# Kernel optimization log

Measured on AMD Instinct MI355X. Metric: run time of the kernel, lower is better.

## Reference

```python
import jax, jax.numpy as jnp
import numpy as np

H = W = 512
IN_DIM = 3
WIDTH = 64
N_LAYERS = 4
M1 = M2 = 20
FC_DIM = 128
OUT_DIM = 1


def setup_inputs() -> dict:
    key = jax.random.key(0)
    ks = jax.random.split(key, 12)
    s = 1.0 / (WIDTH * WIDTH)
    return {
        "x": jax.random.normal(ks[0], (H, W, IN_DIM), jnp.float32),
        "fc0_w": jax.random.normal(ks[1], (WIDTH, IN_DIM), jnp.float32) * 0.1,
        "fc0_b": jnp.zeros((WIDTH,), jnp.float32),
        "sw1_r": jax.random.normal(ks[2], (N_LAYERS, WIDTH, WIDTH, M1, M2), jnp.float32) * s,
        "sw1_i": jax.random.normal(ks[3], (N_LAYERS, WIDTH, WIDTH, M1, M2), jnp.float32) * s,
        "sw2_r": jax.random.normal(ks[4], (N_LAYERS, WIDTH, WIDTH, M1, M2), jnp.float32) * s,
        "sw2_i": jax.random.normal(ks[5], (N_LAYERS, WIDTH, WIDTH, M1, M2), jnp.float32) * s,
        "conv_w": jax.random.normal(ks[6], (N_LAYERS, WIDTH, WIDTH), jnp.float32) * 0.1,
        "conv_b": jnp.zeros((N_LAYERS, WIDTH), jnp.float32),
        "fc1_w": jax.random.normal(ks[7], (FC_DIM, WIDTH), jnp.float32) * 0.1,
        "fc1_b": jnp.zeros((FC_DIM,), jnp.float32),
        "fc2_w": jax.random.normal(ks[8], (OUT_DIM, FC_DIM), jnp.float32) * 0.1,
        "fc2_b": jnp.zeros((OUT_DIM,), jnp.float32),
    }


def _spectral_conv(v, w1, w2):
    # v: (C, H, W); w1, w2: (C_in, C_out, M1, M2) complex64
    xf = jnp.fft.rfft2(v)  # (C, H, W//2+1) complex64
    out_ft = jnp.zeros((w1.shape[1], H, W // 2 + 1), jnp.complex64)
    top = jnp.einsum("ixy,ioxy->oxy", xf[:, :M1, :M2], w1)
    bot = jnp.einsum("ixy,ioxy->oxy", xf[:, -M1:, :M2], w2)
    out_ft = out_ft.at[:, :M1, :M2].set(top).at[:, -M1:, :M2].set(bot)
    return jnp.fft.irfft2(out_ft, s=(H, W))


def reference(x, fc0_w, fc0_b, sw1_r, sw1_i, sw2_r, sw2_i, conv_w, conv_b,
              fc1_w, fc1_b, fc2_w, fc2_b):
    v = jnp.transpose(x, (2, 0, 1))  # (in_dim, H, W)
    # fc0 applied pointwise over the grid (double_vmap Linear on channel axis)
    v = jnp.einsum("chw,oc->ohw", v, fc0_w) + fc0_b[:, None, None]
    for i in range(N_LAYERS):
        w1 = (sw1_r[i] + 1j * sw1_i[i]).astype(jnp.complex64)
        w2 = (sw2_r[i] + 1j * sw2_i[i]).astype(jnp.complex64)
        x1 = _spectral_conv(v, w1, w2)
        x2 = jnp.einsum("chw,oc->ohw", v, conv_w[i]) + conv_b[i][:, None, None]
        v = jnp.tanh(x1 + x2)
    v = jnp.tanh(jnp.einsum("chw,oc->ohw", v, fc1_w) + fc1_b[:, None, None])
    v = jnp.einsum("chw,oc->ohw", v, fc2_w) + fc2_b[:, None, None]
    return jnp.transpose(v, (1, 2, 0))  # (H, W, out_dim)
```

## Files before the change

### kernel.cpp

```cpp
#include <hip/hip_runtime.h>
#include <math.h>

typedef unsigned short u16;
typedef __attribute__((ext_vector_type(8))) short short8;
typedef __attribute__((ext_vector_type(8))) short bf16x8;
typedef __attribute__((ext_vector_type(4))) unsigned short us4;
typedef __attribute__((ext_vector_type(2))) unsigned short us2;
typedef __attribute__((ext_vector_type(4))) float f32x4;

#define NP (512*512)
#define MFMA16 __builtin_amdgcn_mfma_f32_16x16x32_bf16

#define TWH   0u
#define TWL   49152u
#define T2H   98304u
#define T2L   163840u
#define THC2H 229376u
#define THC2L 278528u
#define THS2H 327680u
#define THS2L 376832u
#define THCAH 425984u
#define THCAL 491520u
#define THSAH 557056u
#define THSAL 622592u
#define THSNH 688128u
#define THSNL 753664u
#define CFH   819200u
#define CFL   851968u
#define F1H   884736u
#define F1L   901120u
#define XWH   917504u
#define XWL   4063232u
#define XFP   7208960u
#define YPART 8028160u
#define YRH   8847360u
#define YRL   9011200u
#define YIH   9175040u
#define YIL   9338880u
#define ZH    9502720u
#define ZL    13697024u
#define VH    17891328u
#define VL    51445760u

__device__ __forceinline__ u16 brnd(float x){
    unsigned u = __float_as_uint(x);
    unsigned r = (u + 0x7FFFu + ((u>>16)&1u)) >> 16;
    return (u16)r;
}
__device__ __forceinline__ float fbf(u16 h){ return __uint_as_float(((unsigned)h)<<16); }
__device__ __forceinline__ void bsplit(float x, u16& h, u16& l){
    h = brnd(x); l = brnd(x - fbf(h));
}
__device__ __forceinline__ float tanhfast(float x){
    x = fminf(10.f, fmaxf(-10.f, x));
    float e = __expf(2.f*x);
    return (e-1.f)/(e+1.f);
}

__global__ void k_tables(char* wsb){
    int i = blockIdx.x*256 + threadIdx.x;
    const float c2pi = 6.283185307179586f/512.0f;
    if (i < 24576){
        int e=i&7, lane=(i>>3)&63, g=i>>9; int nt=g%3;
        int k = (g/3)*32 + ((lane>>4)<<3) + e;
        int n = nt*16 + (lane&15);
        float v=0.f;
        if(n<40){int kx=n>>1; float a=c2pi*(float)((kx*k)&511); v=(n&1)?-sinf(a):cosf(a);}
        u16 h,l; bsplit(v,h,l);
        ((u16*)(wsb+TWH))[i]=h; ((u16*)(wsb+TWL))[i]=l;
    } else if (i < 57344){
        int j2=i-24576;
        int e=j2&7, lane=(j2>>3)&63, g=j2>>9; int ks=g&1, wt=g>>1;
        int j = ks*32 + ((lane>>4)<<3) + e;
        int w = wt*16 + (lane&15);
        float v=0.f;
        if(j<40){int kx=j>>1; float a=c2pi*(float)((kx*w)&511); v=(j&1)?-sinf(a):cosf(a);}
        u16 h,l; bsplit(v,h,l);
        ((u16*)(wsb+T2H))[j2]=h; ((u16*)(wsb+T2L))[j2]=l;
    } else if (i < 81920){
        int j2 = i-57344;
        int m=j2>>9, hh=j2&511;
        float vc=0.f,vs=0.f;
        if(m<40){int ky=(m<20)?m:(472+m); float a=c2pi*(float)((ky*hh)&511); vc=cosf(a); vs=sinf(a);}
        u16 h,l;
        bsplit(vc,h,l); ((u16*)(wsb+THC2H))[j2]=h; ((u16*)(wsb+THC2L))[j2]=l;
        bsplit(vs,h,l); ((u16*)(wsb+THS2H))[j2]=h; ((u16*)(wsb+THS2L))[j2]=l;
    } else if (i < 114688){
        int j2 = i-81920;
        int hh=j2>>6, m=j2&63;
        float vc=0.f,vs=0.f;
        if(m<40){int ky=(m<20)?m:(472+m); float a=c2pi*(float)((ky*hh)&511); vc=cosf(a); vs=sinf(a);}
        u16 h,l;
        bsplit(vc,h,l);  ((u16*)(wsb+THCAH))[j2]=h; ((u16*)(wsb+THCAL))[j2]=l;
        bsplit(vs,h,l);  ((u16*)(wsb+THSAH))[j2]=h; ((u16*)(wsb+THSAL))[j2]=l;
        bsplit(-vs,h,l); ((u16*)(wsb+THSNH))[j2]=h; ((u16*)(wsb+THSNL))[j2]=l;
    }
}

__global__ void k_wprep(const float* __restrict__ convw, const float* __restrict__ fc1w, char* wsb){
    int i = blockIdx.x*256 + threadIdx.x;
    if (i < 16384){
        int e=i&7, lane=(i>>3)&63, g=i>>9;
        int mt=g&3, ks=(g>>2)&1, L=g>>3;
        int o = mt*16+(lane&15), c = ks*32+((lane>>4)<<3)+e;
        float v = convw[L*4096 + o*64 + c];
        u16 h,l; bsplit(v,h,l);
        ((u16*)(wsb+CFH))[i]=h; ((u16*)(wsb+CFL))[i]=l;
    } else if (i < 24576){
        int j2=i-16384;
        int e=j2&7, lane=(j2>>3)&63, g=j2>>9;
        int mt=g&7, ks=g>>3;
        int f = mt*16+(lane&15), c = ks*32+((lane>>4)<<3)+e;
        float v = fc1w[f*64+c];
        u16 h,l; bsplit(v,h,l);
        ((u16*)(wsb+F1H))[j2]=h; ((u16*)(wsb+F1L))[j2]=l;
    }
}

__global__ __launch_bounds__(256) void k_fc0(const float* __restrict__ x,
    const float* __restrict__ w, const float* __restrict__ b,
    u16* __restrict__ vh, u16* __restrict__ vl){
    __shared__ float xs[1024*3];
    __shared__ float ws3[192], bs[64];
    int t = threadIdx.x;
    size_t pb = (size_t)blockIdx.x*1024;
    const float4* xg = (const float4*)(x + pb*3);
    float4* xs4 = (float4*)xs;
    #pragma unroll
    for (int k=0;k<3;k++) xs4[t + k*256] = xg[t + k*256];
    if (t<192) ws3[t]=w[t];
    if (t<64) bs[t]=b[t];
    __syncthreads();
    int p0 = t*4;
    float X0[4],X1[4],X2[4];
    #pragma unroll
    for(int e=0;e<4;e++){X0[e]=xs[(p0+e)*3];X1[e]=xs[(p0+e)*3+1];X2[e]=xs[(p0+e)*3+2];}
    for (int c=0;c<64;c++){
        float w0=ws3[c*3],w1=ws3[c*3+1],w2=ws3[c*3+2],bc=bs[c];
        us4 sh, sl;
        #pragma unroll
        for(int e=0;e<4;e++){
            float v = w0*X0[e]+w1*X1[e]+w2*X2[e]+bc;
            u16 hh,ll; bsplit(v,hh,ll); sh[e]=hh; sl[e]=ll;
        }
        *(us4*)(vh + (size_t)c*NP + pb + p0) = sh;
        *(us4*)(vl + (size_t)c*NP + pb + p0) = sl;
    }
}

__global__ __launch_bounds__(256) void k_f1(const u16* __restrict__ vh, const u16* __restrict__ vl,
    const u16* __restrict__ twh, const u16* __restrict__ twl,
    u16* __restrict__ xwh, u16* __restrict__ xwl){
    int lane = threadIdx.x & 63, wv = threadIdx.x >> 6;
    int rowa = blockIdx.x*64 + wv*16 + (lane&15);
    const u16* ah = vh + (size_t)rowa*512 + ((lane>>4)<<3);
    const u16* al = vl + (size_t)rowa*512 + ((lane>>4)<<3);
    f32x4 acc[3];
    #pragma unroll
    for (int nt = 0; nt < 3; ++nt) acc[nt] = (f32x4){0.f,0.f,0.f,0.f};
    for (int kk = 0; kk < 16; ++kk){
        bf16x8 Ah = *reinterpret_cast<const bf16x8*>(ah + kk*32);
        bf16x8 Al = *reinterpret_cast<const bf16x8*>(al + kk*32);
        #pragma unroll
        for (int nt = 0; nt < 3; ++nt){
            size_t bo = ((size_t)(kk*3+nt)*64 + lane)*8;
            bf16x8 Bh = *reinterpret_cast<const bf16x8*>(twh + bo);
            bf16x8 Bl = *reinterpret_cast<const bf16x8*>(twl + bo);
            acc[nt] = MFMA16(Ah, Bh, acc[nt], 0,0,0);
            acc[nt] = MFMA16(Ah, Bl, acc[nt], 0,0,0);
            acc[nt] = MFMA16(Al, Bh, acc[nt], 0,0,0);
        }
    }
    int r0 = blockIdx.x*64 + wv*16 + ((lane>>4)<<2);
    int c = r0>>9, h0 = r0&511;
    int colj = lane&15;
    #pragma unroll
    for (int nt = 0; nt < 3; ++nt){
        int j = nt*16 + colj;
        us4 uh, ul;
        #pragma unroll
        for (int rg = 0; rg < 4; ++rg){
            u16 hh,ll; bsplit(acc[nt][rg],hh,ll); uh[rg]=hh; ul[rg]=ll;
        }
        size_t off = ((size_t)j*64 + c)*512 + h0;
        *(us4*)(xwh + off) = uh;
        *(us4*)(xwl + off) = ul;
    }
}

__global__ __launch_bounds__(256) void k_f2(const char* __restrict__ wsb, float* __restrict__ xfP){
    int b = blockIdx.x; int kx = b>>1, kh = b&1;
    int lane = threadIdx.x&63, wv = threadIdx.x>>6;
    const u16* thch=(const u16*)(wsb+THC2H); const u16* thcl=(const u16*)(wsb+THC2L);
    const u16* thsh=(const u16*)(wsb+THS2H); const u16* thsl=(const u16*)(wsb+THS2L);
    const u16* xwh=(const u16*)(wsb+XWH);   const u16* xwl=(const u16*)(wsb+XWL);
    f32x4 aA[3],aB[3],aC[3],aD[3];
    #pragma unroll
    for(int mt=0;mt<3;mt++){aA[mt]=(f32x4){0,0,0,0};aB[mt]=aA[mt];aC[mt]=aA[mt];aD[mt]=aA[mt];}
    int g8 = (lane>>4)<<3;
    int mrow = lane&15;
    int cB = wv*16 + (lane&15);
    size_t bre = ((size_t)(2*kx)*64 + cB)*512;
    size_t bim = ((size_t)(2*kx+1)*64 + cB)*512;
    for (int kk = kh*8; kk < kh*8+8; ++kk){
        int hof = kk*32 + g8;
        bf16x8 XRh = *reinterpret_cast<const bf16x8*>(xwh + bre + hof);
        bf16x8 XRl = *reinterpret_cast<const bf16x8*>(xwl + bre + hof);
        bf16x8 XIh = *reinterpret_cast<const bf16x8*>(xwh + bim + hof);
        bf16x8 XIl = *reinterpret_cast<const bf16x8*>(xwl + bim + hof);
        #pragma unroll
        for (int mt=0;mt<3;mt++){
            size_t ao = (size_t)(mt*16+mrow)*512 + hof;
            bf16x8 Ch = *reinterpret_cast<const bf16x8*>(thch+ao);
            bf16x8 Cl = *reinterpret_cast<const bf16x8*>(thcl+ao);
            bf16x8 Sh = *reinterpret_cast<const bf16x8*>(thsh+ao);
            bf16x8 Sl = *reinterpret_cast<const bf16x8*>(thsl+ao);
            aA[mt]=MFMA16(Ch,XRh,aA[mt],0,0,0); aA[mt]=MFMA16(Ch,XRl,aA[mt],0,0,0); aA[mt]=MFMA16(Cl,XRh,aA[mt],0,0,0);
            aB[mt]=MFMA16(Sh,XIh,aB[mt],0,0,0); aB[mt]=MFMA16(Sh,XIl,aB[mt],0,0,0); aB[mt]=MFMA16(Sl,XIh,aB[mt],0,0,0);
            aC[mt]=MFMA16(Ch,XIh,aC[mt],0,0,0); aC[mt]=MFMA16(Ch,XIl,aC[mt],0,0,0); aC[mt]=MFMA16(Cl,XIh,aC[mt],0,0,0);
            aD[mt]=MFMA16(Sh,XRh,aD[mt],0,0,0); aD[mt]=MFMA16(Sh,XRl,aD[mt],0,0,0); aD[mt]=MFMA16(Sl,XRh,aD[mt],0,0,0);
        }
    }
    #pragma unroll
    for (int mt=0;mt<3;mt++)
        #pragma unroll
        for (int rg=0;rg<4;rg++){
            int m = mt*16 + ((lane>>4)<<2) + rg;
            if (m < 40){
                float re = aA[mt][rg]+aB[mt][rg];
                float im = aC[mt][rg]-aD[mt][rg];
                size_t xo = ((size_t)kh*64 + cB)*1600 + (size_t)(m*20+kx)*2;
                xfP[xo] = re; xfP[xo+1] = im;
            }
        }
}

__global__ __launch_bounds__(256) void k_mix(const float* __restrict__ w1r,const float* __restrict__ w1i,
    const float* __restrict__ w2r,const float* __restrict__ w2i,
    const float* __restrict__ xfP, float* __restrict__ ypart){
    __shared__ float xs[2][800];
    int b = blockIdx.x;
    int iseg = b>>7, half = (b>>6)&1, o = b&63;
    int t = threadIdx.x;
    const float* wr = (half? w2r : w1r) + o*400;
    const float* wi = (half? w2i : w1i) + o*400;
    const float* xp0 = xfP + half*800;
    const float* xp1 = xfP + (size_t)64*1600 + half*800;
    int i0 = iseg*32;
    {
        const float* a = xp0 + (size_t)i0*1600; const float* c = xp1 + (size_t)i0*1600;
        xs[0][t]=a[t]+c[t]; xs[0][t+256]=a[t+256]+c[t+256];
        if (t<288) xs[0][t+512]=a[t+512]+c[t+512];
    }
    int p1 = t, p2 = t+256; bool has2 = (p2<400);
    float ar1=0,ai1=0,ar2=0,ai2=0;
    size_t wof = (size_t)i0*25600;
    float wAr1=wr[wof+p1], wAi1=wi[wof+p1];
    float wAr2=0,wAi2=0;
    if(has2){ wAr2=wr[wof+p2]; wAi2=wi[wof+p2]; }
    __syncthreads();
    for (int ii=0; ii<32; ++ii){
        int cur = ii&1;
        if (ii<31){
            int i = i0+ii+1;
            const float* a = xp0 + (size_t)i*1600; const float* c = xp1 + (size_t)i*1600;
            float* d = xs[cur^1];
            d[t]=a[t]+c[t]; d[t+256]=a[t+256]+c[t+256];
            if(t<288) d[t+512]=a[t+512]+c[t+512];
        }
        float wBr1=0,wBi1=0,wBr2=0,wBi2=0;
        if (ii<31){
            size_t wo2 = (size_t)(i0+ii+1)*25600;
            wBr1=wr[wo2+p1]; wBi1=wi[wo2+p1];
            if(has2){ wBr2=wr[wo2+p2]; wBi2=wi[wo2+p2]; }
        }
        float xr=xs[cur][2*p1], xi=xs[cur][2*p1+1];
        ar1 += xr*wAr1 - xi*wAi1; ai1 += xr*wAi1 + xi*wAr1;
        if (has2){
            float xr2=xs[cur][2*p2], xi2=xs[cur][2*p2+1];
            ar2 += xr2*wAr2 - xi2*wAi2; ai2 += xr2*wAi2 + xi2*wAr2;
        }
        wAr1=wBr1; wAi1=wBi1; wAr2=wBr2; wAi2=wBi2;
        __syncthreads();
    }
    int mode1 = half*400 + p1;
    size_t y1 = ((size_t)(iseg*800 + mode1)*64 + o)*2;
    ypart[y1]=ar1; ypart[y1+1]=ai1;
    if (has2){
        int mode2 = half*400 + p2;
        size_t y2 = ((size_t)(iseg*800 + mode2)*64 + o)*2;
        ypart[y2]=ar2; ypart[y2+1]=ai2;
    }
}

__global__ void k_mixred(const float* __restrict__ ypart, char* wsb){
    int g = blockIdx.x*256+threadIdx.x;
    int m = g&63, o=(g>>6)&63, kx=g>>12;
    float vr=0.f, vi=0.f;
    if (m<40){
        int mode = m*20+kx;
        size_t i0 = ((size_t)mode*64+o)*2;
        size_t i1 = ((size_t)(800+mode)*64+o)*2;
        float sc = (kx==0?1.f:2.f)*(1.f/262144.f);
        vr = (ypart[i0]+ypart[i1])*sc;
        vi = (ypart[i0+1]+ypart[i1+1])*sc;
    }
    u16 h,l; size_t yo = ((size_t)kx*64+o)*64+m;
    bsplit(vr,h,l); ((u16*)(wsb+YRH))[yo]=h; ((u16*)(wsb+YRL))[yo]=l;
    bsplit(vi,h,l); ((u16*)(wsb+YIH))[yo]=h; ((u16*)(wsb+YIL))[yo]=l;
}

__global__ __launch_bounds__(256) void k_i1(const char* __restrict__ wsb,
    u16* __restrict__ zh, u16* __restrict__ zl){
    int b = blockIdx.x; int kx = b>>3, hb = b&7;
    int lane = threadIdx.x&63, wv = threadIdx.x>>6;
    const u16* thcAh=(const u16*)(wsb+THCAH); const u16* thcAl=(const u16*)(wsb+THCAL);
    const u16* thsAh=(const u16*)(wsb+THSAH); const u16* thsAl=(const u16*)(wsb+THSAL);
    const u16* thsnh=(const u16*)(wsb+THSNH); const u16* thsnl=(const u16*)(wsb+THSNL);
    const u16* yrh=(const u16*)(wsb+YRH); const u16* yrl=(const u16*)(wsb+YRL);
    const u16* yih=(const u16*)(wsb+YIH); const u16* yil=(const u16*)(wsb+YIL);
    f32x4 aR[4], aI[4];
    #pragma unroll
    for(int nt=0;nt<4;nt++){aR[nt]=(f32x4){0,0,0,0}; aI[nt]=aR[nt];}
    int g8 = (lane>>4)<<3;
    int hrow = hb*64 + wv*16 + (lane&15);
    #pragma unroll
    for (int ks=0; ks<2; ++ks){
        size_t ao = (size_t)hrow*64 + ks*32 + g8;
        bf16x8 Ch=*reinterpret_cast<const bf16x8*>(thcAh+ao);
        bf16x8 Cl=*reinterpret_cast<const bf16x8*>(thcAl+ao);
        bf16x8 Sh=*reinterpret_cast<const bf16x8*>(thsAh+ao);
        bf16x8 Sl=*reinterpret_cast<const bf16x8*>(thsAl+ao);
        bf16x8 Nh=*reinterpret_cast<const bf16x8*>(thsnh+ao);
        bf16x8 Nl=*reinterpret_cast<const bf16x8*>(thsnl+ao);
        #pragma unroll
        for (int nt=0; nt<4; ++nt){
            int o = nt*16+(lane&15);
            size_t bo = ((size_t)kx*64+o)*64 + ks*32 + g8;
            bf16x8 Rh=*reinterpret_cast<const bf16x8*>(yrh+bo);
            bf16x8 Rl=*reinterpret_cast<const bf16x8*>(yrl+bo);
            bf16x8 Ih=*reinterpret_cast<const bf16x8*>(yih+bo);
            bf16x8 Il=*reinterpret_cast<const bf16x8*>(yil+bo);
            aR[nt]=MFMA16(Ch,Rh,aR[nt],0,0,0); aR[nt]=MFMA16(Ch,Rl,aR[nt],0,0,0); aR[nt]=MFMA16(Cl,Rh,aR[nt],0,0,0);
            aR[nt]=MFMA16(Nh,Ih,aR[nt],0,0,0); aR[nt]=MFMA16(Nh,Il,aR[nt],0,0,0); aR[nt]=MFMA16(Nl,Ih,aR[nt],0,0,0);
            aI[nt]=MFMA16(Sh,Rh,aI[nt],0,0,0); aI[nt]=MFMA16(Sh,Rl,aI[nt],0,0,0); aI[nt]=MFMA16(Sl,Rh,aI[nt],0,0,0);
            aI[nt]=MFMA16(Ch,Ih,aI[nt],0,0,0); aI[nt]=MFMA16(Ch,Il,aI[nt],0,0,0); aI[nt]=MFMA16(Cl,Ih,aI[nt],0,0,0);
        }
    }
    #pragma unroll
    for (int nt=0;nt<4;nt++)
        #pragma unroll
        for (int rg=0;rg<4;rg++){
            int h = hb*64 + wv*16 + ((lane>>4)<<2) + rg;
            int o = nt*16+(lane&15);
            size_t za = ((size_t)h*64+o)*64 + 2*kx;
            u16 h1,l1,h2,l2;
            bsplit(aR[nt][rg],h1,l1); bsplit(aI[nt][rg],h2,l2);
            us2 sh={h1,h2}, sl={l1,l2};
            *(us2*)(zh+za)=sh; *(us2*)(zl+za)=sl;
        }
}

#define SWZ(c,p) ((c) ^ (((p)&7)<<3))
__global__ __launch_bounds__(256) void k_sct(u16* __restrict__ vh, u16* __restrict__ vl,
    const char* __restrict__ wsb, int L, const float* __restrict__ cb,
    const u16* __restrict__ zh, const u16* __restrict__ zl){
    __shared__ u16 sh_[4096];
    __shared__ u16 sl_[4096];
    int t = threadIdx.x, lane = t&63, wv = t>>6;
    int h = blockIdx.x>>3, pb = (blockIdx.x&7)<<6;
    size_t gbase = (size_t)h*512 + pb;
    {
        int c = t>>2, p0=(t&3)<<4;
        short8 a0 = *(const short8*)(vh + (size_t)c*NP + gbase + p0);
        short8 a1 = *(const short8*)(vh + (size_t)c*NP + gbase + p0+8);
        short8 b0 = *(const short8*)(vl + (size_t)c*NP + gbase + p0);
        short8 b1 = *(const short8*)(vl + (size_t)c*NP + gbase + p0+8);
        #pragma unroll
        for (int e=0;e<8;e++){
            sh_[(p0+e)*64 + SWZ(c,p0+e)] = (u16)a0[e];
            sh_[(p0+8+e)*64 + SWZ(c,p0+8+e)] = (u16)a1[e];
            sl_[(p0+e)*64 + SWZ(c,p0+e)] = (u16)b0[e];
            sl_[(p0+8+e)*64 + SWZ(c,p0+8+e)] = (u16)b1[e];
        }
    }
    __syncthreads();
    f32x4 acc[4];
    #pragma unroll
    for (int mt=0;mt<4;mt++) acc[mt]=(f32x4){0,0,0,0};
    int colp = wv*16 + (lane&15);
    int g = lane>>4;
    const u16* cfh=(const u16*)(wsb+CFH); const u16* cfl=(const u16*)(wsb+CFL);
    const u16* t2h=(const u16*)(wsb+T2H); const u16* t2l=(const u16*)(wsb+T2L);
    #pragma unroll
    for (int ks=0;ks<2;ks++){
        int o8 = ks*4+g;
        int so = colp*64 + ((o8 ^ (colp&7))<<3);
        bf16x8 Bh = *reinterpret_cast<const bf16x8*>(sh_+so);
        bf16x8 Bl = *reinterpret_cast<const bf16x8*>(sl_+so);
        #pragma unroll
        for (int mt=0;mt<4;mt++){
            size_t fo = (size_t)(((L*2+ks)*4+mt)*64 + lane)*8;
            bf16x8 Ah = *reinterpret_cast<const bf16x8*>(cfh+fo);
            bf16x8 Al = *reinterpret_cast<const bf16x8*>(cfl+fo);
            acc[mt]=MFMA16(Ah,Bh,acc[mt],0,0,0);
            acc[mt]=MFMA16(Ah,Bl,acc[mt],0,0,0);
            acc[mt]=MFMA16(Al,Bh,acc[mt],0,0,0);
        }
    }
    int wt = (pb>>4) + wv;
    #pragma unroll
    for (int ks=0;ks<2;ks++){
        size_t bo = ((size_t)(wt*2+ks)*64 + lane)*8;
        bf16x8 Bh = *reinterpret_cast<const bf16x8*>(t2h+bo);
        bf16x8 Bl = *reinterpret_cast<const bf16x8*>(t2l+bo);
        #pragma unroll
        for (int mt=0;mt<4;mt++){
            size_t ao = (((size_t)h*64 + mt*16+(lane&15))*64) + ks*32 + (g<<3);
            bf16x8 Ah = *reinterpret_cast<const bf16x8*>(zh+ao);
            bf16x8 Al = *reinterpret_cast<const bf16x8*>(zl+ao);
            acc[mt]=MFMA16(Ah,Bh,acc[mt],0,0,0);
            acc[mt]=MFMA16(Ah,Bl,acc[mt],0,0,0);
            acc[mt]=MFMA16(Al,Bh,acc[mt],0,0,0);
        }
    }
    size_t pg = gbase + colp;
    #pragma unroll
    for (int mt=0;mt<4;mt++)
        #pragma unroll
        for (int rg=0;rg<4;rg++){
            int o = mt*16 + (g<<2) + rg;
            float val = tanhfast(acc[mt][rg] + cb[o]);
            u16 hh,ll; bsplit(val,hh,ll);
            vh[(size_t)o*NP + pg]=hh; vl[(size_t)o*NP + pg]=ll;
        }
}

__global__ __launch_bounds__(256) void k_fc12(const u16* __restrict__ vh, const u16* __restrict__ vl,
    const char* __restrict__ wsb, const float* __restrict__ b1,
    const float* __restrict__ w2, const float* __restrict__ b2, float* __restrict__ out){
    __shared__ u16 sh_[4096];
    __shared__ u16 sl_[4096];
    int t = threadIdx.x, lane = t&63, wv = t>>6;
    size_t pb = (size_t)blockIdx.x*64;
    {
        int c = t>>2, p0=(t&3)<<4;
        short8 a0 = *(const short8*)(vh + (size_t)c*NP + pb + p0);
        short8 a1 = *(const short8*)(vh + (size_t)c*NP + pb + p0+8);
        short8 b0 = *(const short8*)(vl + (size_t)c*NP + pb + p0);
        short8 b1 = *(const short8*)(vl + (size_t)c*NP + pb + p0+8);
        #pragma unroll
        for (int e=0;e<8;e++){
            sh_[(p0+e)*64 + SWZ(c,p0+e)] = (u16)a0[e];
            sh_[(p0+8+e)*64 + SWZ(c,p0+8+e)] = (u16)a1[e];
            sl_[(p0+e)*64 + SWZ(c,p0+e)] = (u16)b0[e];
            sl_[(p0+8+e)*64 + SWZ(c,p0+8+e)] = (u16)b1[e];
        }
    }
    __syncthreads();
    f32x4 acc[8];
    #pragma unroll
    for (int mt=0;mt<8;mt++) acc[mt]=(f32x4){0,0,0,0};
    int colp = wv*16 + (lane&15);
    int g = lane>>4;
    const u16* f1h=(const u16*)(wsb+F1H); const u16* f1l=(const u16*)(wsb+F1L);
    #pragma unroll
    for (int ks=0;ks<2;ks++){
        int o8 = ks*4+g;
        int so = colp*64 + ((o8 ^ (colp&7))<<3);
        bf16x8 Bh = *reinterpret_cast<const bf16x8*>(sh_+so);
        bf16x8 Bl = *reinterpret_cast<const bf16x8*>(sl_+so);
        #pragma unroll
        for (int mt=0;mt<8;mt++){
            size_t fo = (size_t)((ks*8+mt)*64 + lane)*8;
            bf16x8 Ah = *reinterpret_cast<const bf16x8*>(f1h+fo);
            bf16x8 Al = *reinterpret_cast<const bf16x8*>(f1l+fo);
            acc[mt]=MFMA16(Ah,Bh,acc[mt],0,0,0);
            acc[mt]=MFMA16(Ah,Bl,acc[mt],0,0,0);
            acc[mt]=MFMA16(Al,Bh,acc[mt],0,0,0);
        }
    }
    float s = 0.f;
    #pragma unroll
    for (int mt=0;mt<8;mt++)
        #pragma unroll
        for (int rg=0;rg<4;rg++){
            int f = mt*16 + (g<<2) + rg;
            s += w2[f] * tanhfast(acc[mt][rg] + b1[f]);
        }
    s += __shfl_xor(s, 16);
    s += __shfl_xor(s, 32);
    if (lane < 16) out[pb + wv*16 + lane] = s + b2[0];
}

extern "C" void kernel_launch(void* const* d_in, const int* in_sizes, int n_in,
                              void* d_out, int out_size, void* d_ws, size_t ws_size,
                              hipStream_t stream) {
    const float* x     = (const float*)d_in[0];
    const float* fc0w  = (const float*)d_in[1];
    const float* fc0b  = (const float*)d_in[2];
    const float* sw1r  = (const float*)d_in[3];
    const float* sw1i  = (const float*)d_in[4];
    const float* sw2r  = (const float*)d_in[5];
    const float* sw2i  = (const float*)d_in[6];
    const float* convw = (const float*)d_in[7];
    const float* convb = (const float*)d_in[8];
    const float* fc1w  = (const float*)d_in[9];
    const float* fc1b  = (const float*)d_in[10];
    const float* fc2w  = (const float*)d_in[11];
    const float* fc2b  = (const float*)d_in[12];
    char* wsb = (char*)d_ws;
    float* out = (float*)d_out;

    u16* twh = (u16*)(wsb+TWH); u16* twl = (u16*)(wsb+TWL);
    u16* xwh = (u16*)(wsb+XWH); u16* xwl = (u16*)(wsb+XWL);
    float* xfP = (float*)(wsb+XFP);
    float* ypart = (float*)(wsb+YPART);
    u16* zh = (u16*)(wsb+ZH); u16* zl = (u16*)(wsb+ZL);
    u16* vh = (u16*)(wsb+VH); u16* vl = (u16*)(wsb+VL);

    k_tables<<<448, 256, 0, stream>>>(wsb);
    k_wprep<<<96, 256, 0, stream>>>(convw, fc1w, wsb);
    k_fc0<<<256, 256, 0, stream>>>(x, fc0w, fc0b, vh, vl);
    for (int L = 0; L < 4; ++L){
        size_t so = (size_t)L * 64 * 64 * 400;
        k_f1<<<512, 256, 0, stream>>>(vh, vl, twh, twl, xwh, xwl);
        k_f2<<<40, 256, 0, stream>>>(wsb, xfP);
        k_mix<<<256, 256, 0, stream>>>(sw1r+so, sw1i+so, sw2r+so, sw2i+so, xfP, ypart);
        k_mixred<<<320, 256, 0, stream>>>(ypart, wsb);
        k_i1<<<160, 256, 0, stream>>>(wsb, zh, zl);
        k_sct<<<4096, 256, 0, stream>>>(vh, vl, wsb, L, convb + (size_t)L*64, zh, zl);
    }
    k_fc12<<<4096, 256, 0, stream>>>(vh, vl, wsb, fc1b, fc2w, fc2b, out);
}
```

Baseline: 806.2 us.

## Split f2/i1 grids wider, coalesce sct stores via LDS, hoist MFMA operand loads

```diff
diff --git a/kernel.cpp b/kernel.cpp
--- a/kernel.cpp
+++ b/kernel.cpp
@@ -6,6 +6,7 @@
 typedef __attribute__((ext_vector_type(8))) short bf16x8;
 typedef __attribute__((ext_vector_type(4))) unsigned short us4;
 typedef __attribute__((ext_vector_type(2))) unsigned short us2;
+typedef __attribute__((ext_vector_type(8))) unsigned short us8;
 typedef __attribute__((ext_vector_type(4))) float f32x4;
 
 #define NP (512*512)
@@ -57,7 +58,7 @@
     return (e-1.f)/(e+1.f);
 }
 
-__global__ void k_tables(char* wsb){
+__global__ void k_setup(char* wsb, const float* __restrict__ convw, const float* __restrict__ fc1w){
     int i = blockIdx.x*256 + threadIdx.x;
     const float c2pi = 6.283185307179586f/512.0f;
     if (i < 24576){
@@ -94,26 +95,24 @@
         bsplit(vc,h,l);  ((u16*)(wsb+THCAH))[j2]=h; ((u16*)(wsb+THCAL))[j2]=l;
         bsplit(vs,h,l);  ((u16*)(wsb+THSAH))[j2]=h; ((u16*)(wsb+THSAL))[j2]=l;
         bsplit(-vs,h,l); ((u16*)(wsb+THSNH))[j2]=h; ((u16*)(wsb+THSNL))[j2]=l;
-    }
-}
-
-__global__ void k_wprep(const float* __restrict__ convw, const float* __restrict__ fc1w, char* wsb){
-    int i = blockIdx.x*256 + threadIdx.x;
-    if (i < 16384){
-        int e=i&7, lane=(i>>3)&63, g=i>>9;
-        int mt=g&3, ks=(g>>2)&1, L=g>>3;
-        int o = mt*16+(lane&15), c = ks*32+((lane>>4)<<3)+e;
-        float v = convw[L*4096 + o*64 + c];
-        u16 h,l; bsplit(v,h,l);
-        ((u16*)(wsb+CFH))[i]=h; ((u16*)(wsb+CFL))[i]=l;
-    } else if (i < 24576){
-        int j2=i-16384;
-        int e=j2&7, lane=(j2>>3)&63, g=j2>>9;
-        int mt=g&7, ks=g>>3;
-        int f = mt*16+(lane&15), c = ks*32+((lane>>4)<<3)+e;
-        float v = fc1w[f*64+c];
-        u16 h,l; bsplit(v,h,l);
-        ((u16*)(wsb+F1H))[j2]=h; ((u16*)(wsb+F1L))[j2]=l;
+    } else {
+        int j = i - 114688;
+        if (j < 16384){
+            int e=j&7, lane=(j>>3)&63, g=j>>9;
+            int mt=g&3, ks=(g>>2)&1, L=g>>3;
+            int o = mt*16+(lane&15), c = ks*32+((lane>>4)<<3)+e;
+            float v = convw[L*4096 + o*64 + c];
+            u16 h,l; bsplit(v,h,l);
+            ((u16*)(wsb+CFH))[j]=h; ((u16*)(wsb+CFL))[j]=l;
+        } else {
+            int j2=j-16384;
+            int e=j2&7, lane=(j2>>3)&63, g=j2>>9;
+            int mt=g&7, ks=g>>3;
+            int f = mt*16+(lane&15), c = ks*32+((lane>>4)<<3)+e;
+            float v = fc1w[f*64+c];
+            u16 h,l; bsplit(v,h,l);
+            ((u16*)(wsb+F1H))[j2]=h; ((u16*)(wsb+F1L))[j2]=l;
+        }
     }
 }
 
@@ -158,17 +157,22 @@
     f32x4 acc[3];
     #pragma unroll
     for (int nt = 0; nt < 3; ++nt) acc[nt] = (f32x4){0.f,0.f,0.f,0.f};
+    #pragma unroll 2
     for (int kk = 0; kk < 16; ++kk){
         bf16x8 Ah = *reinterpret_cast<const bf16x8*>(ah + kk*32);
         bf16x8 Al = *reinterpret_cast<const bf16x8*>(al + kk*32);
+        bf16x8 Bh[3], Bl[3];
         #pragma unroll
         for (int nt = 0; nt < 3; ++nt){
             size_t bo = ((size_t)(kk*3+nt)*64 + lane)*8;
-            bf16x8 Bh = *reinterpret_cast<const bf16x8*>(twh + bo);
-            bf16x8 Bl = *reinterpret_cast<const bf16x8*>(twl + bo);
-            acc[nt] = MFMA16(Ah, Bh, acc[nt], 0,0,0);
-            acc[nt] = MFMA16(Ah, Bl, acc[nt], 0,0,0);
-            acc[nt] = MFMA16(Al, Bh, acc[nt], 0,0,0);
+            Bh[nt] = *reinterpret_cast<const bf16x8*>(twh + bo);
+            Bl[nt] = *reinterpret_cast<const bf16x8*>(twl + bo);
+        }
+        #pragma unroll
+        for (int nt = 0; nt < 3; ++nt){
+            acc[nt] = MFMA16(Ah, Bh[nt], acc[nt], 0,0,0);
+            acc[nt] = MFMA16(Ah, Bl[nt], acc[nt], 0,0,0);
+            acc[nt] = MFMA16(Al, Bh[nt], acc[nt], 0,0,0);
         }
     }
     int r0 = blockIdx.x*64 + wv*16 + ((lane>>4)<<2);
@@ -189,14 +193,13 @@
 }
 
 __global__ __launch_bounds__(256) void k_f2(const char* __restrict__ wsb, float* __restrict__ xfP){
-    int b = blockIdx.x; int kx = b>>1, kh = b&1;
+    int b = blockIdx.x;
+    int kx = b/6, r = b%6, mt = r>>1, kh = r&1;
     int lane = threadIdx.x&63, wv = threadIdx.x>>6;
     const u16* thch=(const u16*)(wsb+THC2H); const u16* thcl=(const u16*)(wsb+THC2L);
     const u16* thsh=(const u16*)(wsb+THS2H); const u16* thsl=(const u16*)(wsb+THS2L);
     const u16* xwh=(const u16*)(wsb+XWH);   const u16* xwl=(const u16*)(wsb+XWL);
-    f32x4 aA[3],aB[3],aC[3],aD[3];
-    #pragma unroll
-    for(int mt=0;mt<3;mt++){aA[mt]=(f32x4){0,0,0,0};aB[mt]=aA[mt];aC[mt]=aA[mt];aD[mt]=aA[mt];}
+    f32x4 aA=(f32x4){0,0,0,0}, aB=aA, aC=aA, aD=aA;
     int g8 = (lane>>4)<<3;
     int mrow = lane&15;
     int cB = wv*16 + (lane&15);
@@ -208,31 +211,26 @@
         bf16x8 XRl = *reinterpret_cast<const bf16x8*>(xwl + bre + hof);
         bf16x8 XIh = *reinterpret_cast<const bf16x8*>(xwh + bim + hof);
         bf16x8 XIl = *reinterpret_cast<const bf16x8*>(xwl + bim + hof);
-        #pragma unroll
-        for (int mt=0;mt<3;mt++){
-            size_t ao = (size_t)(mt*16+mrow)*512 + hof;
-            bf16x8 Ch = *reinterpret_cast<const bf16x8*>(thch+ao);
-            bf16x8 Cl = *reinterpret_cast<const bf16x8*>(thcl+ao);
-            bf16x8 Sh = *reinterpret_cast<const bf16x8*>(thsh+ao);
-            bf16x8 Sl = *reinterpret_cast<const bf16x8*>(thsl+ao);
-            aA[mt]=MFMA16(Ch,XRh,aA[mt],0,0,0); aA[mt]=MFMA16(Ch,XRl,aA[mt],0,0,0); aA[mt]=MFMA16(Cl,XRh,aA[mt],0,0,0);
-            aB[mt]=MFMA16(Sh,XIh,aB[mt],0,0,0); aB[mt]=MFMA16(Sh,XIl,aB[mt],0,0,0); aB[mt]=MFMA16(Sl,XIh,aB[mt],0,0,0);
-            aC[mt]=MFMA16(Ch,XIh,aC[mt],0,0,0); aC[mt]=MFMA16(Ch,XIl,aC[mt],0,0,0); aC[mt]=MFMA16(Cl,XIh,aC[mt],0,0,0);
-            aD[mt]=MFMA16(Sh,XRh,aD[mt],0,0,0); aD[mt]=MFMA16(Sh,XRl,aD[mt],0,0,0); aD[mt]=MFMA16(Sl,XRh,aD[mt],0,0,0);
-        }
-    }
-    #pragma unroll
-    for (int mt=0;mt<3;mt++)
-        #pragma unroll
-        for (int rg=0;rg<4;rg++){
-            int m = mt*16 + ((lane>>4)<<2) + rg;
-            if (m < 40){
-                float re = aA[mt][rg]+aB[mt][rg];
-                float im = aC[mt][rg]-aD[mt][rg];
-                size_t xo = ((size_t)kh*64 + cB)*1600 + (size_t)(m*20+kx)*2;
-                xfP[xo] = re; xfP[xo+1] = im;
-            }
-        }
+        size_t ao = (size_t)(mt*16+mrow)*512 + hof;
+        bf16x8 Ch = *reinterpret_cast<const bf16x8*>(thch+ao);
+        bf16x8 Cl = *reinterpret_cast<const bf16x8*>(thcl+ao);
+        bf16x8 Sh = *reinterpret_cast<const bf16x8*>(thsh+ao);
+        bf16x8 Sl = *reinterpret_cast<const bf16x8*>(thsl+ao);
+        aA=MFMA16(Ch,XRh,aA,0,0,0); aA=MFMA16(Ch,XRl,aA,0,0,0); aA=MFMA16(Cl,XRh,aA,0,0,0);
+        aB=MFMA16(Sh,XIh,aB,0,0,0); aB=MFMA16(Sh,XIl,aB,0,0,0); aB=MFMA16(Sl,XIh,aB,0,0,0);
+        aC=MFMA16(Ch,XIh,aC,0,0,0); aC=MFMA16(Ch,XIl,aC,0,0,0); aC=MFMA16(Cl,XIh,aC,0,0,0);
+        aD=MFMA16(Sh,XRh,aD,0,0,0); aD=MFMA16(Sh,XRl,aD,0,0,0); aD=MFMA16(Sl,XRh,aD,0,0,0);
+    }
+    #pragma unroll
+    for (int rg=0;rg<4;rg++){
+        int m = mt*16 + ((lane>>4)<<2) + rg;
+        if (m < 40){
+            float re = aA[rg]+aB[rg];
+            float im = aC[rg]-aD[rg];
+            size_t xo = ((size_t)kh*64 + cB)*1600 + (size_t)(m*20+kx)*2;
+            xfP[xo] = re; xfP[xo+1] = im;
+        }
+    }
 }
 
 __global__ __launch_bounds__(256) void k_mix(const float* __restrict__ w1r,const float* __restrict__ w1i,
@@ -310,9 +308,9 @@
     bsplit(vi,h,l); ((u16*)(wsb+YIH))[yo]=h; ((u16*)(wsb+YIL))[yo]=l;
 }
 
-__global__ __launch_bounds__(256) void k_i1(const char* __restrict__ wsb,
+__global__ __launch_bounds__(128) void k_i1(const char* __restrict__ wsb,
     u16* __restrict__ zh, u16* __restrict__ zl){
-    int b = blockIdx.x; int kx = b>>3, hb = b&7;
+    int b = blockIdx.x; int kx = b>>4, hb = b&15;
     int lane = threadIdx.x&63, wv = threadIdx.x>>6;
     const u16* thcAh=(const u16*)(wsb+THCAH); const u16* thcAl=(const u16*)(wsb+THCAL);
     const u16* thsAh=(const u16*)(wsb+THSAH); const u16* thsAl=(const u16*)(wsb+THSAL);
@@ -323,7 +321,7 @@
     #pragma unroll
     for(int nt=0;nt<4;nt++){aR[nt]=(f32x4){0,0,0,0}; aI[nt]=aR[nt];}
     int g8 = (lane>>4)<<3;
-    int hrow = hb*64 + wv*16 + (lane&15);
+    int hrow = hb*32 + wv*16 + (lane&15);
     #pragma unroll
     for (int ks=0; ks<2; ++ks){
         size_t ao = (size_t)hrow*64 + ks*32 + g8;
@@ -351,7 +349,7 @@
     for (int nt=0;nt<4;nt++)
         #pragma unroll
         for (int rg=0;rg<4;rg++){
-            int h = hb*64 + wv*16 + ((lane>>4)<<2) + rg;
+            int h = hb*32 + wv*16 + ((lane>>4)<<2) + rg;
             int o = nt*16+(lane&15);
             size_t za = ((size_t)h*64+o)*64 + 2*kx;
             u16 h1,l1,h2,l2;
@@ -367,73 +365,135 @@
     const u16* __restrict__ zh, const u16* __restrict__ zl){
     __shared__ u16 sh_[4096];
     __shared__ u16 sl_[4096];
+    __shared__ unsigned so_[64*68];
     int t = threadIdx.x, lane = t&63, wv = t>>6;
     int h = blockIdx.x>>3, pb = (blockIdx.x&7)<<6;
     size_t gbase = (size_t)h*512 + pb;
-    {
-        int c = t>>2, p0=(t&3)<<4;
-        short8 a0 = *(const short8*)(vh + (size_t)c*NP + gbase + p0);
-        short8 a1 = *(const short8*)(vh + (size_t)c*NP + gbase + p0+8);
-        short8 b0 = *(const short8*)(vl + (size_t)c*NP + gbase + p0);
-        short8 b1 = *(const short8*)(vl + (size_t)c*NP + gbase + p0+8);
-        #pragma unroll
-        for (int e=0;e<8;e++){
-            sh_[(p0+e)*64 + SWZ(c,p0+e)] = (u16)a0[e];
-            sh_[(p0+8+e)*64 + SWZ(c,p0+8+e)] = (u16)a1[e];
-            sl_[(p0+e)*64 + SWZ(c,p0+e)] = (u16)b0[e];
-            sl_[(p0+8+e)*64 + SWZ(c,p0+8+e)] = (u16)b1[e];
-        }
+    const u16* cfh=(const u16*)(wsb+CFH); const u16* cfl=(const u16*)(wsb+CFL);
+    const u16* t2h=(const u16*)(wsb+T2H); const u16* t2l=(const u16*)(wsb+T2L);
+    int g = lane>>4;
+    int colp = wv*16 + (lane&15);
+    int wt = (pb>>4) + wv;
+    int cst = t>>2, p0s=(t&3)<<4;
+    short8 a0 = *(const short8*)(vh + (size_t)cst*NP + gbase + p0s);
+    short8 a1 = *(const short8*)(vh + (size_t)cst*NP + gbase + p0s+8);
+    short8 b0 = *(const short8*)(vl + (size_t)cst*NP + gbase + p0s);
+    short8 b1 = *(const short8*)(vl + (size_t)cst*NP + gbase + p0s+8);
+    bf16x8 cA0[4][2], zA0[4][2], tB0[2];
+    #pragma unroll
+    for (int mt=0;mt<4;mt++){
+        size_t fo = (size_t)(((L*2+0)*4+mt)*64 + lane)*8;
+        cA0[mt][0] = *reinterpret_cast<const bf16x8*>(cfh+fo);
+        cA0[mt][1] = *reinterpret_cast<const bf16x8*>(cfl+fo);
+        size_t ao = (((size_t)h*64 + mt*16+(lane&15))*64) + (g<<3);
+        zA0[mt][0] = *reinterpret_cast<const bf16x8*>(zh+ao);
+        zA0[mt][1] = *reinterpret_cast<const bf16x8*>(zl+ao);
+    }
+    {
+        size_t bo = ((size_t)(wt*2+0)*64 + lane)*8;
+        tB0[0] = *reinterpret_cast<const bf16x8*>(t2h+bo);
+        tB0[1] = *reinterpret_cast<const bf16x8*>(t2l+bo);
+    }
+    #pragma unroll
+    for (int e=0;e<8;e++){
+        sh_[(p0s+e)*64 + SWZ(cst,p0s+e)] = (u16)a0[e];
+        sh_[(p0s+8+e)*64 + SWZ(cst,p0s+8+e)] = (u16)a1[e];
+        sl_[(p0s+e)*64 + SWZ(cst,p0s+e)] = (u16)b0[e];
+        sl_[(p0s+8+e)*64 + SWZ(cst,p0s+8+e)] = (u16)b1[e];
     }
     __syncthreads();
     f32x4 acc[4];
     #pragma unroll
     for (int mt=0;mt<4;mt++) acc[mt]=(f32x4){0,0,0,0};
-    int colp = wv*16 + (lane&15);
-    int g = lane>>4;
-    const u16* cfh=(const u16*)(wsb+CFH); const u16* cfl=(const u16*)(wsb+CFL);
-    const u16* t2h=(const u16*)(wsb+T2H); const u16* t2l=(const u16*)(wsb+T2L);
-    #pragma unroll
-    for (int ks=0;ks<2;ks++){
-        int o8 = ks*4+g;
-        int so = colp*64 + ((o8 ^ (colp&7))<<3);
+    {
+        int so = colp*64 + ((g ^ (colp&7))<<3);
         bf16x8 Bh = *reinterpret_cast<const bf16x8*>(sh_+so);
         bf16x8 Bl = *reinterpret_cast<const bf16x8*>(sl_+so);
         #pragma unroll
         for (int mt=0;mt<4;mt++){
-            size_t fo = (size_t)(((L*2+ks)*4+mt)*64 + lane)*8;
-            bf16x8 Ah = *reinterpret_cast<const bf16x8*>(cfh+fo);
-            bf16x8 Al = *reinterpret_cast<const bf16x8*>(cfl+fo);
-            acc[mt]=MFMA16(Ah,Bh,acc[mt],0,0,0);
-            acc[mt]=MFMA16(Ah,Bl,acc[mt],0,0,0);
-            acc[mt]=MFMA16(Al,Bh,acc[mt],0,0,0);
-        }
-    }
-    int wt = (pb>>4) + wv;
-    #pragma unroll
-    for (int ks=0;ks<2;ks++){
-        size_t bo = ((size_t)(wt*2+ks)*64 + lane)*8;
-        bf16x8 Bh = *reinterpret_cast<const bf16x8*>(t2h+bo);
-        bf16x8 Bl = *reinterpret_cast<const bf16x8*>(t2l+bo);
+            acc[mt]=MFMA16(cA0[mt][0],Bh,acc[mt],0,0,0);
+            acc[mt]=MFMA16(cA0[mt][0],Bl,acc[mt],0,0,0);
+            acc[mt]=MFMA16(cA0[mt][1],Bh,acc[mt],0,0,0);
+        }
+    }
+    bf16x8 cA1[4][2], zA1[4][2], tB1[2];
+    #pragma unroll
+    for (int mt=0;mt<4;mt++){
+        size_t fo = (size_t)(((L*2+1)*4+mt)*64 + lane)*8;
+        cA1[mt][0] = *reinterpret_cast<const bf16x8*>(cfh+fo);
+        cA1[mt][1] = *reinterpret_cast<const bf16x8*>(cfl+fo);
+        size_t ao = (((size_t)h*64 + mt*16+(lane&15))*64) + 32 + (g<<3);
+        zA1[mt][0] = *reinterpret_cast<const bf16x8*>(zh+ao);
+        zA1[mt][1] = *reinterpret_cast<const bf16x8*>(zl+ao);
+    }
+    {
+        size_t bo = ((size_t)(wt*2+1)*64 + lane)*8;
+        tB1[0] = *reinterpret_cast<const bf16x8*>(t2h+bo);
+        tB1[1] = *reinterpret_cast<const bf16x8*>(t2l+bo);
+    }
+    #pragma unroll
+    for (int mt=0;mt<4;mt++){
+        acc[mt]=MFMA16(zA0[mt][0],tB0[0],acc[mt],0,0,0);
+        acc[mt]=MFMA16(zA0[mt][0],tB0[1],acc[mt],0,0,0);
+        acc[mt]=MFMA16(zA0[mt][1],tB0[0],acc[mt],0,0,0);
+    }
+    {
+        int so = colp*64 + (((4+g) ^ (colp&7))<<3);
+        bf16x8 Bh = *reinterpret_cast<const bf16x8*>(sh_+so);
+        bf16x8 Bl = *reinterpret_cast<const bf16x8*>(sl_+so);
         #pragma unroll
         for (int mt=0;mt<4;mt++){
-            size_t ao = (((size_t)h*64 + mt*16+(lane&15))*64) + ks*32 + (g<<3);
-            bf16x8 Ah = *reinterpret_cast<const bf16x8*>(zh+ao);
-            bf16x8 Al = *reinterpret_cast<const bf16x8*>(zl+ao);
-            acc[mt]=MFMA16(Ah,Bh,acc[mt],0,0,0);
-            acc[mt]=MFMA16(Ah,Bl,acc[mt],0,0,0);
-            acc[mt]=MFMA16(Al,Bh,acc[mt],0,0,0);
-        }
-    }
-    size_t pg = gbase + colp;
-    #pragma unroll
-    for (int mt=0;mt<4;mt++)
+            acc[mt]=MFMA16(cA1[mt][0],Bh,acc[mt],0,0,0);
+            acc[mt]=MFMA16(cA1[mt][0],Bl,acc[mt],0,0,0);
+            acc[mt]=MFMA16(cA1[mt][1],Bh,acc[mt],0,0,0);
+        }
+    }
+    #pragma unroll
+    for (int mt=0;mt<4;mt++){
+        acc[mt]=MFMA16(zA1[mt][0],tB1[0],acc[mt],0,0,0);
+        acc[mt]=MFMA16(zA1[mt][0],tB1[1],acc[mt],0,0,0);
+        acc[mt]=MFMA16(zA1[mt][1],tB1[0],acc[mt],0,0,0);
+    }
+    #pragma unroll
+    for (int mt=0;mt<4;mt++){
+        float4 cbv = *reinterpret_cast<const float4*>(cb + mt*16 + (g<<2));
+        float cba[4] = {cbv.x, cbv.y, cbv.z, cbv.w};
         #pragma unroll
         for (int rg=0;rg<4;rg++){
             int o = mt*16 + (g<<2) + rg;
-            float val = tanhfast(acc[mt][rg] + cb[o]);
+            float val = tanhfast(acc[mt][rg] + cba[rg]);
             u16 hh,ll; bsplit(val,hh,ll);
-            vh[(size_t)o*NP + pg]=hh; vl[(size_t)o*NP + pg]=ll;
-        }
+            so_[o*68 + colp] = (unsigned)hh | ((unsigned)ll<<16);
+        }
+    }
+    __syncthreads();
+    {
+        int o = t>>2, p0 = (t&3)<<4;
+        const uint4* sp = reinterpret_cast<const uint4*>(so_ + o*68 + p0);
+        uint4 u0 = sp[0], u1 = sp[1], u2 = sp[2], u3 = sp[3];
+        us8 h0, h1, l0, l1;
+        h0[0]=(u16)u0.x; l0[0]=(u16)(u0.x>>16);
+        h0[1]=(u16)u0.y; l0[1]=(u16)(u0.y>>16);
+        h0[2]=(u16)u0.z; l0[2]=(u16)(u0.z>>16);
+        h0[3]=(u16)u0.w; l0[3]=(u16)(u0.w>>16);
+        h0[4]=(u16)u1.x; l0[4]=(u16)(u1.x>>16);
+        h0[5]=(u16)u1.y; l0[5]=(u16)(u1.y>>16);
+        h0[6]=(u16)u1.z; l0[6]=(u16)(u1.z>>16);
+        h0[7]=(u16)u1.w; l0[7]=(u16)(u1.w>>16);
+        h1[0]=(u16)u2.x; l1[0]=(u16)(u2.x>>16);
+        h1[1]=(u16)u2.y; l1[1]=(u16)(u2.y>>16);
+        h1[2]=(u16)u2.z; l1[2]=(u16)(u2.z>>16);
+        h1[3]=(u16)u2.w; l1[3]=(u16)(u2.w>>16);
+        h1[4]=(u16)u3.x; l1[4]=(u16)(u3.x>>16);
+        h1[5]=(u16)u3.y; l1[5]=(u16)(u3.y>>16);
+        h1[6]=(u16)u3.z; l1[6]=(u16)(u3.z>>16);
+        h1[7]=(u16)u3.w; l1[7]=(u16)(u3.w>>16);
+        size_t go = (size_t)o*NP + gbase + p0;
+        *(us8*)(vh+go)   = h0;
+        *(us8*)(vh+go+8) = h1;
+        *(us8*)(vl+go)   = l0;
+        *(us8*)(vl+go+8) = l1;
+    }
 }
 
 __global__ __launch_bounds__(256) void k_fc12(const u16* __restrict__ vh, const u16* __restrict__ vl,
@@ -466,18 +526,22 @@
     const u16* f1h=(const u16*)(wsb+F1H); const u16* f1l=(const u16*)(wsb+F1L);
     #pragma unroll
     for (int ks=0;ks<2;ks++){
+        bf16x8 A[8][2];
+        #pragma unroll
+        for (int mt=0;mt<8;mt++){
+            size_t fo = (size_t)((ks*8+mt)*64 + lane)*8;
+            A[mt][0] = *reinterpret_cast<const bf16x8*>(f1h+fo);
+            A[mt][1] = *reinterpret_cast<const bf16x8*>(f1l+fo);
+        }
         int o8 = ks*4+g;
         int so = colp*64 + ((o8 ^ (colp&7))<<3);
         bf16x8 Bh = *reinterpret_cast<const bf16x8*>(sh_+so);
         bf16x8 Bl = *reinterpret_cast<const bf16x8*>(sl_+so);
         #pragma unroll
         for (int mt=0;mt<8;mt++){
-            size_t fo = (size_t)((ks*8+mt)*64 + lane)*8;
-            bf16x8 Ah = *reinterpret_cast<const bf16x8*>(f1h+fo);
-            bf16x8 Al = *reinterpret_cast<const bf16x8*>(f1l+fo);
-            acc[mt]=MFMA16(Ah,Bh,acc[mt],0,0,0);
-            acc[mt]=MFMA16(Ah,Bl,acc[mt],0,0,0);
-            acc[mt]=MFMA16(Al,Bh,acc[mt],0,0,0);
+            acc[mt]=MFMA16(A[mt][0],Bh,acc[mt],0,0,0);
+            acc[mt]=MFMA16(A[mt][0],Bl,acc[mt],0,0,0);
+            acc[mt]=MFMA16(A[mt][1],Bh,acc[mt],0,0,0);
         }
     }
     float s = 0.f;
@@ -519,16 +583,15 @@
     u16* zh = (u16*)(wsb+ZH); u16* zl = (u16*)(wsb+ZL);
     u16* vh = (u16*)(wsb+VH); u16* vl = (u16*)(wsb+VL);
 
-    k_tables<<<448, 256, 0, stream>>>(wsb);
-    k_wprep<<<96, 256, 0, stream>>>(convw, fc1w, wsb);
+    k_setup<<<544, 256, 0, stream>>>(wsb, convw, fc1w);
     k_fc0<<<256, 256, 0, stream>>>(x, fc0w, fc0b, vh, vl);
     for (int L = 0; L < 4; ++L){
         size_t so = (size_t)L * 64 * 64 * 400;
         k_f1<<<512, 256, 0, stream>>>(vh, vl, twh, twl, xwh, xwl);
-        k_f2<<<40, 256, 0, stream>>>(wsb, xfP);
+        k_f2<<<120, 256, 0, stream>>>(wsb, xfP);
         k_mix<<<256, 256, 0, stream>>>(sw1r+so, sw1i+so, sw2r+so, sw2i+so, xfP, ypart);
         k_mixred<<<320, 256, 0, stream>>>(ypart, wsb);
-        k_i1<<<160, 256, 0, stream>>>(wsb, zh, zl);
+        k_i1<<<320, 128, 0, stream>>>(wsb, zh, zl);
         k_sct<<<4096, 256, 0, stream>>>(vh, vl, wsb, L, convb + (size_t)L*64, zh, zl);
     }
     k_fc12<<<4096, 256, 0, stream>>>(vh, vl, wsb, fc1b, fc2w, fc2b, out);
```

Result: faster. 729.4 us (-9.5%).
